# Kernel optimization log

Hardware: AMD Instinct MI355X
Metric: run time of the kernel (lower is better)

Reference implementation:

```python
import jax, jax.numpy as jnp
import numpy as np

N = 20000        # nodes
E = 320000       # edges (avg degree 16)
F_IN = 128       # node_features
F2 = 64          # second_features (per-head out dim, LSTM hidden)
H = 8            # heads
D1 = H * F2      # 512, concat output of GATConv / LSTM input
NEG_SLOPE = 0.2  # GATConv default leaky_relu slope


def _gat_conv(x, src, dst, W, att_src, att_dst, bias):
    """PyG GATConv (concat=True, self-loops added, eval-mode dropout)."""
    n = x.shape[0]
    h = (x @ W).reshape(n, H, -1)                      # [N,H,F]
    a_s = (h * att_src).sum(-1)                        # [N,H]
    a_d = (h * att_dst).sum(-1)                        # [N,H]
    e = jax.nn.leaky_relu(a_s[src] + a_d[dst], NEG_SLOPE)   # [E',H]
    m = jax.ops.segment_max(e, dst, num_segments=n)    # [N,H]
    m = jnp.where(jnp.isfinite(m), m, 0.0)
    ex = jnp.exp(e - m[dst])
    denom = jax.ops.segment_sum(ex, dst, num_segments=n)
    alpha = ex / (denom[dst] + 1e-16)                  # [E',H]
    msg = h[src] * alpha[:, :, None]                   # [E',H,F]
    out = jax.ops.segment_sum(msg, dst, num_segments=n)  # [N,H,F]
    return out.reshape(n, -1) + bias                   # [N,H*F]


def _lstm_step(x, W_ih, W_hh, b_ih, b_hh):
    """Single-timestep PyTorch LSTM with zero initial (h0, c0). x: [N,D1]."""
    h0 = jnp.zeros((x.shape[0], F2), x.dtype)
    gates = x @ W_ih.T + b_ih + h0 @ W_hh.T + b_hh     # [N,4*F2]
    i, f, g, o = jnp.split(gates, 4, axis=-1)
    c = jax.nn.sigmoid(f) * 0.0 + jax.nn.sigmoid(i) * jnp.tanh(g)
    h = jax.nn.sigmoid(o) * jnp.tanh(c)
    return h, (h, c)


def setup_inputs() -> dict:
    key = jax.random.key(0)
    ks = jax.random.split(key, 16)

    def glorot(k, shape, fan_in):
        return jax.random.normal(k, shape, jnp.float32) * (1.0 / np.sqrt(fan_in))

    return {
        "x": jax.random.normal(ks[0], (N, F_IN), jnp.float32),
        "edge_index": jax.random.randint(ks[1], (2, E), 0, N, jnp.int32),
        "edge_weight": jax.random.uniform(ks[2], (E,), jnp.float32),
        # GATConv 1: F_IN -> H*F2
        "W1": glorot(ks[3], (F_IN, H * F2), F_IN),
        "att_src1": glorot(ks[4], (H, F2), F2),
        "att_dst1": glorot(ks[5], (H, F2), F2),
        "bias1": jnp.zeros((H * F2,), jnp.float32),
        # LSTM: input D1 -> hidden F2
        "W_ih": glorot(ks[6], (4 * F2, D1), D1),
        "W_hh": glorot(ks[7], (4 * F2, F2), F2),
        "b_ih": jnp.zeros((4 * F2,), jnp.float32),
        "b_hh": jnp.zeros((4 * F2,), jnp.float32),
        # GATConv 2: F2 -> H*F2
        "W2": glorot(ks[8], (F2, H * F2), F2),
        "att_src2": glorot(ks[9], (H, F2), F2),
        "att_dst2": glorot(ks[10], (H, F2), F2),
        "bias2": jnp.zeros((H * F2,), jnp.float32),
    }


def reference(x, edge_index, edge_weight, W1, att_src1, att_dst1, bias1,
              W_ih, W_hh, b_ih, b_hh, W2, att_src2, att_dst2, bias2):
    # edge_weight is accepted but unused, matching the original forward.
    loops = jnp.arange(N, dtype=edge_index.dtype)
    src = jnp.concatenate([edge_index[0], loops])      # add self-loops (PyG default)
    dst = jnp.concatenate([edge_index[1], loops])

    h = _gat_conv(x, src, dst, W1, att_src1, att_dst1, bias1)   # [N,512]
    h, hidden2 = _lstm_step(h, W_ih, W_hh, b_ih, b_hh)          # [N,64]
    h = jax.nn.relu(h)
    h = _gat_conv(h, src, dst, W2, att_src2, att_dst2, bias2)   # [N,512]
    return jax.nn.softmax(h, axis=1)
```

## Files before the change

kernel.cpp:

```cpp
#include <hip/hip_runtime.h>
#include <math.h>


__global__ void count_kernel(const int* __restrict__ dst, int* __restrict__ deg, int E) {
  int i = blockIdx.x * 256 + threadIdx.x;
  if (i < E) atomicAdd(&deg[dst[i]], 1);
}

__global__ void scan_kernel(const int* __restrict__ deg, int* __restrict__ rowptr, int n) {
  __shared__ int buf[1024];
  __shared__ int carry;
  if (threadIdx.x == 0) carry = 0;
  __syncthreads();
  for (int base = 0; base < n; base += 8192) {
    int v[8];
    int tsum = 0;
    int i0 = base + (int)threadIdx.x * 8;
#pragma unroll
    for (int k = 0; k < 8; ++k) {
      int i = i0 + k;
      v[k] = (i < n) ? (deg[i] + 1) : 0;
      tsum += v[k];
    }
    int incl = tsum;
    buf[threadIdx.x] = incl;
    __syncthreads();
    for (int s = 1; s < 1024; s <<= 1) {
      int t = (threadIdx.x >= (unsigned)s) ? buf[threadIdx.x - s] : 0;
      __syncthreads();
      incl += t;
      buf[threadIdx.x] = incl;
      __syncthreads();
    }
    int excl = carry + incl - tsum;
#pragma unroll
    for (int k = 0; k < 8; ++k) {
      int i = i0 + k;
      if (i < n) rowptr[i] = excl;
      excl += v[k];
    }
    int total = buf[1023];
    __syncthreads();
    if (threadIdx.x == 0) carry += total;
    __syncthreads();
  }
  if (threadIdx.x == 0) rowptr[n] = carry;
}

__global__ void scatter_kernel(const int* __restrict__ src, const int* __restrict__ dst,
                               const int* __restrict__ rowptr, int* __restrict__ wp,
                               int* __restrict__ col, int E, int n) {
  int i = blockIdx.x * 256 + threadIdx.x;
  if (i < E) {
    int d = dst[i];
    int p = rowptr[d] + atomicAdd(&wp[d], 1);
    col[p] = src[i];
  } else if (i < E + n) {
    int d = i - E;
    int p = rowptr[d] + atomicAdd(&wp[d], 1);
    col[p] = d;
  }
}


template <int BMt>
__global__ __launch_bounds__(256) void gemm_kernel(
    const float* __restrict__ A, const float* __restrict__ B,
    float* __restrict__ C, const float* __restrict__ bias,
    int M, int K, int lda, int ldb, int ldc,
    int aZ, int bZ, int cZ, int biasZ) {
  constexpr int BNt = 64, BKt = 16;
  constexpr int TM = BMt / 16;
  constexpr int AST = (BMt * BKt) / (256 * 4);
  __shared__ float As[BKt][BMt + 4];
  __shared__ float Bs[BKt][BNt];
  const int z = blockIdx.z;
  A += (size_t)z * aZ;
  B += (size_t)z * bZ;
  C += (size_t)z * cZ;
  const int tid = threadIdx.x;
  const int bm = blockIdx.y * BMt;
  const int bn = blockIdx.x * BNt;
  const int tm = (tid >> 4) * TM;
  const int tn = (tid & 15) * 4;
  int arow_[AST], akq_[AST];
#pragma unroll
  for (int i = 0; i < AST; ++i) {
    int idx = tid + i * 256;
    arow_[i] = idx >> 2;
    akq_[i] = (idx & 3) * 4;
  }
  const int bk = tid >> 4, bn4 = (tid & 15) * 4;
  float4 pa[AST], pb;
#pragma unroll
  for (int i = 0; i < AST; ++i) {
    pa[i] = make_float4(0.f, 0.f, 0.f, 0.f);
    if (bm + arow_[i] < M)
      pa[i] = *reinterpret_cast<const float4*>(A + (size_t)(bm + arow_[i]) * lda + akq_[i]);
  }
  pb = *reinterpret_cast<const float4*>(B + (size_t)bk * ldb + bn + bn4);
  float acc[TM][4] = {};
  for (int k0 = 0; k0 < K; k0 += BKt) {
#pragma unroll
    for (int i = 0; i < AST; ++i) {
      As[akq_[i] + 0][arow_[i]] = pa[i].x; As[akq_[i] + 1][arow_[i]] = pa[i].y;
      As[akq_[i] + 2][arow_[i]] = pa[i].z; As[akq_[i] + 3][arow_[i]] = pa[i].w;
    }
    *reinterpret_cast<float4*>(&Bs[bk][bn4]) = pb;
    __syncthreads();
    const int kn = k0 + BKt;
    if (kn < K) {
#pragma unroll
      for (int i = 0; i < AST; ++i) {
        float4 t = make_float4(0.f, 0.f, 0.f, 0.f);
        if (bm + arow_[i] < M)
          t = *reinterpret_cast<const float4*>(A + (size_t)(bm + arow_[i]) * lda + kn + akq_[i]);
        pa[i] = t;
      }
      pb = *reinterpret_cast<const float4*>(B + (size_t)(kn + bk) * ldb + bn + bn4);
    }
#pragma unroll
    for (int k = 0; k < BKt; ++k) {
      float a[TM], b[4];
#pragma unroll
      for (int i = 0; i < TM; ++i) a[i] = As[k][tm + i];
#pragma unroll
      for (int j = 0; j < 4; ++j) b[j] = Bs[k][tn + j];
#pragma unroll
      for (int i = 0; i < TM; ++i)
#pragma unroll
        for (int j = 0; j < 4; ++j) acc[i][j] = fmaf(a[i], b[j], acc[i][j]);
    }
    __syncthreads();
  }
  float4 bz = make_float4(0.f, 0.f, 0.f, 0.f);
  if (bias) bz = *reinterpret_cast<const float4*>(bias + (size_t)z * biasZ + bn + tn);
#pragma unroll
  for (int i = 0; i < TM; ++i) {
    int m = bm + tm + i;
    if (m < M) {
      float4 o;
      o.x = acc[i][0] + bz.x; o.y = acc[i][1] + bz.y;
      o.z = acc[i][2] + bz.z; o.w = acc[i][3] + bz.w;
      *reinterpret_cast<float4*>(C + (size_t)m * ldc + bn + tn) = o;
    }
  }
}


__global__ void prep_all_kernel(const float* __restrict__ W_ih, const float* __restrict__ b_ih,
                                const float* __restrict__ b_hh, const float* __restrict__ W1,
                                const float* __restrict__ as1, const float* __restrict__ ad1,
                                const float* __restrict__ W2, const float* __restrict__ as2,
                                const float* __restrict__ ad2, float* __restrict__ Wt,
                                float* __restrict__ bsum, float* __restrict__ watt1,
                                float* __restrict__ watt2) {
  int idx = blockIdx.x * 256 + threadIdx.x;
  if (idx < 98304) {
    int k = idx / 192, jp = idx - k * 192;
    int j = (jp < 64) ? jp : jp + 64;
    Wt[idx] = W_ih[(size_t)j * 512 + k];
  } else if (idx < 98496) {
    int jp = idx - 98304;
    int j = (jp < 64) ? jp : jp + 64;
    bsum[jp] = b_ih[j] + b_hh[j];
  } else if (idx < 100544) {
    int t = idx - 98496;
    int f = t >> 4, c = t & 15;
    int k = c & 7;
    const float* att = ((c < 8) ? as1 : ad1) + k * 64;
    const float* w = W1 + (size_t)f * 512 + k * 64;
    float s = 0.f;
#pragma unroll
    for (int j = 0; j < 64; ++j) s = fmaf(w[j], att[j], s);
    watt1[t] = s;
  } else if (idx < 101568) {
    int t = idx - 100544;
    int f = t >> 4, c = t & 15;
    int k = c & 7;
    const float* att = ((c < 8) ? as2 : ad2) + k * 64;
    const float* w = W2 + (size_t)f * 512 + k * 64;
    float s = 0.f;
#pragma unroll
    for (int j = 0; j < 64; ++j) s = fmaf(w[j], att[j], s);
    watt2[t] = s;
  }
}


template <int F>
__global__ __launch_bounds__(256) void attcoef_kernel(
    const float* __restrict__ feat, const float* __restrict__ watt,
    float* __restrict__ a_s, float* __restrict__ a_d, int n) {
  __shared__ float rows[16 * F];
  __shared__ float wbuf[F * 16];
  const int n0 = blockIdx.x * 16;
  const int tid = threadIdx.x;
  if (n0 + 16 <= n) {
    const float4* g = reinterpret_cast<const float4*>(feat + (size_t)n0 * F);
    float4* l = reinterpret_cast<float4*>(rows);
    for (int i = tid; i < 16 * F / 4; i += 256) l[i] = g[i];
  } else {
    for (int i = tid; i < 16 * F; i += 256) {
      int r = i / F;
      rows[i] = (n0 + r < n) ? feat[(size_t)(n0 + r) * F + (i - r * F)] : 0.f;
    }
  }
  {
    const float4* g = reinterpret_cast<const float4*>(watt);
    float4* l = reinterpret_cast<float4*>(wbuf);
    for (int i = tid; i < F * 16 / 4; i += 256) l[i] = g[i];
  }
  __syncthreads();
  const int local = tid >> 4, c = tid & 15;
  float s = 0.f;
#pragma unroll 8
  for (int f = 0; f < F; ++f) s = fmaf(rows[local * F + f], wbuf[f * 16 + c], s);
  const int node = n0 + local;
  if (node < n) {
    if (c < 8) a_s[(size_t)node * 8 + c] = s;
    else       a_d[(size_t)node * 8 + (c - 8)] = s;
  }
}


template <int F>
__global__ __launch_bounds__(256) void gat_aggregate_wave(
    const float* __restrict__ feat, const float* __restrict__ a_s,
    const float* __restrict__ a_d, const int* __restrict__ rowptr,
    const int* __restrict__ col, float* __restrict__ agg, int n) {
  constexpr int F4 = F / 4;
  constexpr int HPG = (F == 128) ? 4 : 2;
  __shared__ float s_alpha[4][8][8];
  __shared__ int s_cols[4][8];
  const int wid = threadIdx.x >> 6;
  const int lane = threadIdx.x & 63;
  const int node = blockIdx.x * 4 + wid;
  if (node >= n) return;
  const int start = rowptr[node];
  const int deg = rowptr[node + 1] - start;
  const int j = lane >> 3;
  const int h = lane & 7;
  const float adh = a_d[(size_t)node * 8 + h];
  float den = 0.f;
  for (int e = j; e < deg; e += 8) {
    int s = col[start + e];
    float v = a_s[(size_t)s * 8 + h] + adh;
    v = (v > 0.f) ? v : 0.2f * v;
    den += __expf(v);
  }
  den += __shfl_xor(den, 8);
  den += __shfl_xor(den, 16);
  den += __shfl_xor(den, 32);
  const float inv = 1.f / (den + 1e-16f);
  const int f4 = lane & (F4 - 1);
  const int hbase = (lane / F4) * HPG;
  float4 acc0 = make_float4(0.f, 0.f, 0.f, 0.f);
  float4 acc1 = make_float4(0.f, 0.f, 0.f, 0.f);
  float4 acc2 = make_float4(0.f, 0.f, 0.f, 0.f);
  float4 acc3 = make_float4(0.f, 0.f, 0.f, 0.f);
  for (int c0 = 0; c0 < deg; c0 += 8) {
    float aval = 0.f;
    int sj = 0;
    if (c0 + j < deg) {
      sj = col[start + c0 + j];
      float v = a_s[(size_t)sj * 8 + h] + adh;
      v = (v > 0.f) ? v : 0.2f * v;
      aval = __expf(v) * inv;
    }
    s_alpha[wid][j][h] = aval;
    if (h == 0) s_cols[wid][j] = sj;
    __builtin_amdgcn_wave_barrier();
    const int ce = min(8, deg - c0);
    for (int e = 0; e < ce; ++e) {
      int s = s_cols[wid][e];
      float4 fv = *reinterpret_cast<const float4*>(feat + (size_t)s * F + f4 * 4);
      if constexpr (HPG == 4) {
        float4 al = *reinterpret_cast<const float4*>(&s_alpha[wid][e][hbase]);
        acc0.x = fmaf(al.x, fv.x, acc0.x); acc0.y = fmaf(al.x, fv.y, acc0.y);
        acc0.z = fmaf(al.x, fv.z, acc0.z); acc0.w = fmaf(al.x, fv.w, acc0.w);
        acc1.x = fmaf(al.y, fv.x, acc1.x); acc1.y = fmaf(al.y, fv.y, acc1.y);
        acc1.z = fmaf(al.y, fv.z, acc1.z); acc1.w = fmaf(al.y, fv.w, acc1.w);
        acc2.x = fmaf(al.z, fv.x, acc2.x); acc2.y = fmaf(al.z, fv.y, acc2.y);
        acc2.z = fmaf(al.z, fv.z, acc2.z); acc2.w = fmaf(al.z, fv.w, acc2.w);
        acc3.x = fmaf(al.w, fv.x, acc3.x); acc3.y = fmaf(al.w, fv.y, acc3.y);
        acc3.z = fmaf(al.w, fv.z, acc3.z); acc3.w = fmaf(al.w, fv.w, acc3.w);
      } else {
        float2 al = *reinterpret_cast<const float2*>(&s_alpha[wid][e][hbase]);
        acc0.x = fmaf(al.x, fv.x, acc0.x); acc0.y = fmaf(al.x, fv.y, acc0.y);
        acc0.z = fmaf(al.x, fv.z, acc0.z); acc0.w = fmaf(al.x, fv.w, acc0.w);
        acc1.x = fmaf(al.y, fv.x, acc1.x); acc1.y = fmaf(al.y, fv.y, acc1.y);
        acc1.z = fmaf(al.y, fv.z, acc1.z); acc1.w = fmaf(al.y, fv.w, acc1.w);
      }
    }
    __builtin_amdgcn_wave_barrier();
  }
  float* outp = agg + (size_t)node * 8 * F + (size_t)hbase * F + f4 * 4;
  *reinterpret_cast<float4*>(outp) = acc0;
  *reinterpret_cast<float4*>(outp + F) = acc1;
  if constexpr (HPG == 4) {
    *reinterpret_cast<float4*>(outp + 2 * F) = acc2;
    *reinterpret_cast<float4*>(outp + 3 * F) = acc3;
  }
}


__global__ __launch_bounds__(256) void lstm_act_attcoef_kernel(
    const float* __restrict__ gp0, const float* __restrict__ bsum,
    const float* __restrict__ watt2, float* __restrict__ h2,
    float* __restrict__ a_s2, float* __restrict__ a_d2, int n) {
  __shared__ float h2t[4][64];
  __shared__ float wbuf[64 * 16];
  const int tid = threadIdx.x;
  reinterpret_cast<float4*>(wbuf)[tid] = reinterpret_cast<const float4*>(watt2)[tid];
  const int nl = tid >> 6, j = tid & 63;
  const int node = blockIdx.x * 4 + nl;
  const float* gp1 = gp0 + (size_t)n * 192;
  float hv = 0.f;
  if (node < n) {
    const float* g0 = gp0 + (size_t)node * 192;
    const float* g1 = gp1 + (size_t)node * 192;
    float iv = g0[j] + g1[j] + bsum[j];
    float gv = g0[64 + j] + g1[64 + j] + bsum[64 + j];
    float ov = g0[128 + j] + g1[128 + j] + bsum[128 + j];
    float c = (1.f / (1.f + __expf(-iv))) * tanhf(gv);
    hv = fmaxf((1.f / (1.f + __expf(-ov))) * tanhf(c), 0.f);
    h2[(size_t)node * 64 + j] = hv;
  }
  h2t[nl][j] = hv;
  __syncthreads();
  if (j < 16 && node < n) {
    float s = 0.f;
#pragma unroll 16
    for (int f = 0; f < 64; ++f) s = fmaf(h2t[nl][f], wbuf[f * 16 + j], s);
    if (j < 8) a_s2[(size_t)node * 8 + j] = s;
    else       a_d2[(size_t)node * 8 + (j - 8)] = s;
  }
}


__global__ __launch_bounds__(256) void softmax512_wave(const float* __restrict__ in,
                                                       float* __restrict__ out, int n) {
  const int wid = threadIdx.x >> 6, lane = threadIdx.x & 63;
  const int node = blockIdx.x * 4 + wid;
  if (node >= n) return;
  const float4* ip = reinterpret_cast<const float4*>(in + (size_t)node * 512);
  float4 v0 = ip[lane];
  float4 v1 = ip[64 + lane];
  float m = fmaxf(fmaxf(fmaxf(v0.x, v0.y), fmaxf(v0.z, v0.w)),
                  fmaxf(fmaxf(v1.x, v1.y), fmaxf(v1.z, v1.w)));
#pragma unroll
  for (int d = 1; d < 64; d <<= 1) m = fmaxf(m, __shfl_xor(m, d));
  float4 e0, e1;
  e0.x = __expf(v0.x - m); e0.y = __expf(v0.y - m);
  e0.z = __expf(v0.z - m); e0.w = __expf(v0.w - m);
  e1.x = __expf(v1.x - m); e1.y = __expf(v1.y - m);
  e1.z = __expf(v1.z - m); e1.w = __expf(v1.w - m);
  float s = e0.x + e0.y + e0.z + e0.w + e1.x + e1.y + e1.z + e1.w;
#pragma unroll
  for (int d = 1; d < 64; d <<= 1) s += __shfl_xor(s, d);
  float inv = 1.f / s;
  e0.x *= inv; e0.y *= inv; e0.z *= inv; e0.w *= inv;
  e1.x *= inv; e1.y *= inv; e1.z *= inv; e1.w *= inv;
  float4* op = reinterpret_cast<float4*>(out + (size_t)node * 512);
  op[lane] = e0;
  op[64 + lane] = e1;
}


extern "C" void kernel_launch(void* const* d_in, const int* in_sizes, int n_in,
                              void* d_out, int out_size, void* d_ws, size_t ws_size,
                              hipStream_t stream) {
  const float* x      = (const float*)d_in[0];
  const int*   ei     = (const int*)d_in[1];
  const float* W1     = (const float*)d_in[3];
  const float* att_s1 = (const float*)d_in[4];
  const float* att_d1 = (const float*)d_in[5];
  const float* bias1  = (const float*)d_in[6];
  const float* W_ih   = (const float*)d_in[7];
  const float* b_ih   = (const float*)d_in[9];
  const float* b_hh   = (const float*)d_in[10];
  const float* W2     = (const float*)d_in[11];
  const float* att_s2 = (const float*)d_in[12];
  const float* att_d2 = (const float*)d_in[13];
  const float* bias2  = (const float*)d_in[14];
  float* out = (float*)d_out;

  const int N = in_sizes[0] / 128;
  const int E = in_sizes[1] / 2;
  const int* src = ei;
  const int* dst = ei + E;

  char* p = (char*)d_ws;
  auto alloc = [&](size_t bytes) {
    char* r = p;
    p += (bytes + 255) & ~(size_t)255;
    return r;
  };
  float* slotA = (float*)alloc((size_t)N * 1024 * 4);
  float* slotB = (float*)alloc((size_t)N * 512 * 4);
  float* a_s1 = (float*)alloc((size_t)N * 8 * 4);
  float* a_d1 = (float*)alloc((size_t)N * 8 * 4);
  float* a_s2 = (float*)alloc((size_t)N * 8 * 4);
  float* a_d2 = (float*)alloc((size_t)N * 8 * 4);
  float* watt1 = (float*)alloc(128 * 16 * 4);
  float* watt2 = (float*)alloc(64 * 16 * 4);
  float* Wt   = (float*)alloc((size_t)512 * 192 * 4);
  float* bsum = (float*)alloc(192 * 4);
  int* deg    = (int*)alloc((size_t)2 * N * 4);
  int* wp     = deg + N;
  int* rowptr = (int*)alloc((size_t)(N + 1) * 4);
  int* col    = (int*)alloc((size_t)(E + N) * 4);

  float* agg1   = slotA;
  float* g1     = slotB;
  float* gates2 = slotA;
  float* h2     = slotA + (size_t)N * 384;
  float* agg2   = slotA + (size_t)N * 448;
  float* h3p    = slotB;

  hipMemsetAsync(deg, 0, (size_t)2 * N * 4, stream);
  count_kernel<<<(E + 255) / 256, 256, 0, stream>>>(dst, deg, E);
  scan_kernel<<<1, 1024, 0, stream>>>(deg, rowptr, N);
  scatter_kernel<<<(E + N + 255) / 256, 256, 0, stream>>>(src, dst, rowptr, wp, col, E, N);

  prep_all_kernel<<<(101568 + 255) / 256, 256, 0, stream>>>(
      W_ih, b_ih, b_hh, W1, att_s1, att_d1, W2, att_s2, att_d2,
      Wt, bsum, watt1, watt2);

  attcoef_kernel<128><<<(N + 15) / 16, 256, 0, stream>>>(x, watt1, a_s1, a_d1, N);
  gat_aggregate_wave<128><<<(N + 3) / 4, 256, 0, stream>>>(x, a_s1, a_d1, rowptr, col, agg1, N);
  {
    dim3 g(1, (N + 127) / 128, 8);
    gemm_kernel<128><<<g, 256, 0, stream>>>(agg1, W1, g1, bias1,
                                            N, 128, 1024, 512, 512, 128, 64, 64, 64);
  }

  {
    dim3 g(3, (N + 63) / 64, 2);
    gemm_kernel<64><<<g, 256, 0, stream>>>(g1, Wt, gates2, nullptr,
                                           N, 256, 512, 192, 192,
                                           256, 256 * 192, N * 192, 0);
  }
  lstm_act_attcoef_kernel<<<(N + 3) / 4, 256, 0, stream>>>(gates2, bsum, watt2,
                                                           h2, a_s2, a_d2, N);

  gat_aggregate_wave<64><<<(N + 3) / 4, 256, 0, stream>>>(h2, a_s2, a_d2, rowptr, col, agg2, N);
  {
    dim3 g(1, (N + 127) / 128, 8);
    gemm_kernel<128><<<g, 256, 0, stream>>>(agg2, W2, h3p, bias2,
                                            N, 64, 512, 512, 512, 64, 64, 64, 64);
  }
  softmax512_wave<<<(N + 3) / 4, 256, 0, stream>>>(h3p, out, N);
}
```

Measured before the change: 388.4 us.

## Fold W1 into LSTM input weights and fuse two GEMMs into one

Precomputes a fused weight matrix (per-head W1 slice times W_ih) so the aggregated features go straight to LSTM gates through a single K=1024 GEMM. This removes the intermediate g1 buffer and one GEMM launch, and folds bias1 into the gate bias. The GEMM gets wider N tiles (192 columns), and the K dimension is split into 2 or 4 parts depending on workspace size. It also drops the memset by zeroing degrees in the prep kernel and simplifies the scan to a single pass. In exchange the K split adds partial-sum traffic and the FLOP count rises from K=128+512 to K=1024 per node.

```diff
diff --git a/kernel.cpp b/kernel.cpp
--- a/kernel.cpp
+++ b/kernel.cpp
@@ -9,42 +9,34 @@
 
 __global__ void scan_kernel(const int* __restrict__ deg, int* __restrict__ rowptr, int n) {
   __shared__ int buf[1024];
-  __shared__ int carry;
-  if (threadIdx.x == 0) carry = 0;
+  const int tid = threadIdx.x;
+  const int i0 = tid * 20;
+  int v[20];
+  int tsum = 0;
+#pragma unroll
+  for (int k = 0; k < 20; ++k) {
+    int i = i0 + k;
+    v[k] = (i < n) ? (deg[i] + 1) : 0;
+    tsum += v[k];
+  }
+  int incl = tsum;
+  buf[tid] = incl;
   __syncthreads();
-  for (int base = 0; base < n; base += 8192) {
-    int v[8];
-    int tsum = 0;
-    int i0 = base + (int)threadIdx.x * 8;
-#pragma unroll
-    for (int k = 0; k < 8; ++k) {
-      int i = i0 + k;
-      v[k] = (i < n) ? (deg[i] + 1) : 0;
-      tsum += v[k];
-    }
-    int incl = tsum;
-    buf[threadIdx.x] = incl;
+  for (int s = 1; s < 1024; s <<= 1) {
+    int t = (tid >= (unsigned)s) ? buf[tid - s] : 0;
     __syncthreads();
-    for (int s = 1; s < 1024; s <<= 1) {
-      int t = (threadIdx.x >= (unsigned)s) ? buf[threadIdx.x - s] : 0;
-      __syncthreads();
-      incl += t;
-      buf[threadIdx.x] = incl;
-      __syncthreads();
-    }
-    int excl = carry + incl - tsum;
-#pragma unroll
-    for (int k = 0; k < 8; ++k) {
-      int i = i0 + k;
-      if (i < n) rowptr[i] = excl;
-      excl += v[k];
-    }
-    int total = buf[1023];
+    incl += t;
+    buf[tid] = incl;
     __syncthreads();
-    if (threadIdx.x == 0) carry += total;
-    __syncthreads();
-  }
-  if (threadIdx.x == 0) rowptr[n] = carry;
+  }
+  int excl = incl - tsum;
+#pragma unroll
+  for (int k = 0; k < 20; ++k) {
+    int i = i0 + k;
+    if (i < n) rowptr[i] = excl;
+    excl += v[k];
+  }
+  if (tid == 1023) rowptr[n] = incl;
 }
 
 __global__ void scatter_kernel(const int* __restrict__ src, const int* __restrict__ dst,
@@ -63,15 +55,17 @@
 }
 
 
-template <int BMt>
+template <int BMt, int BNt, int TNt>
 __global__ __launch_bounds__(256) void gemm_kernel(
     const float* __restrict__ A, const float* __restrict__ B,
     float* __restrict__ C, const float* __restrict__ bias,
     int M, int K, int lda, int ldb, int ldc,
     int aZ, int bZ, int cZ, int biasZ) {
-  constexpr int BNt = 64, BKt = 16;
+  constexpr int BKt = 16;
   constexpr int TM = BMt / 16;
-  constexpr int AST = (BMt * BKt) / (256 * 4);
+  constexpr int AST = (BMt * BKt) / 1024;
+  constexpr int BST = (BKt * BNt) / 1024;
+  static_assert(BNt == 16 * TNt, "layout");
   __shared__ float As[BKt][BMt + 4];
   __shared__ float Bs[BKt][BNt];
   const int z = blockIdx.z;
@@ -82,7 +76,7 @@
   const int bm = blockIdx.y * BMt;
   const int bn = blockIdx.x * BNt;
   const int tm = (tid >> 4) * TM;
-  const int tn = (tid & 15) * 4;
+  const int tn = (tid & 15) * TNt;
   int arow_[AST], akq_[AST];
 #pragma unroll
   for (int i = 0; i < AST; ++i) {
@@ -90,23 +84,33 @@
     arow_[i] = idx >> 2;
     akq_[i] = (idx & 3) * 4;
   }
-  const int bk = tid >> 4, bn4 = (tid & 15) * 4;
-  float4 pa[AST], pb;
+  int bkr_[BST], bc4_[BST];
+#pragma unroll
+  for (int i = 0; i < BST; ++i) {
+    int idx = tid + i * 256;
+    bkr_[i] = idx / (BNt / 4);
+    bc4_[i] = (idx % (BNt / 4)) * 4;
+  }
+  float4 pa[AST], pb[BST];
 #pragma unroll
   for (int i = 0; i < AST; ++i) {
     pa[i] = make_float4(0.f, 0.f, 0.f, 0.f);
     if (bm + arow_[i] < M)
       pa[i] = *reinterpret_cast<const float4*>(A + (size_t)(bm + arow_[i]) * lda + akq_[i]);
   }
-  pb = *reinterpret_cast<const float4*>(B + (size_t)bk * ldb + bn + bn4);
-  float acc[TM][4] = {};
+#pragma unroll
+  for (int i = 0; i < BST; ++i)
+    pb[i] = *reinterpret_cast<const float4*>(B + (size_t)bkr_[i] * ldb + bn + bc4_[i]);
+  float acc[TM][TNt] = {};
   for (int k0 = 0; k0 < K; k0 += BKt) {
 #pragma unroll
     for (int i = 0; i < AST; ++i) {
       As[akq_[i] + 0][arow_[i]] = pa[i].x; As[akq_[i] + 1][arow_[i]] = pa[i].y;
       As[akq_[i] + 2][arow_[i]] = pa[i].z; As[akq_[i] + 3][arow_[i]] = pa[i].w;
     }
-    *reinterpret_cast<float4*>(&Bs[bk][bn4]) = pb;
+#pragma unroll
+    for (int i = 0; i < BST; ++i)
+      *reinterpret_cast<float4*>(&Bs[bkr_[i]][bc4_[i]]) = pb[i];
     __syncthreads();
     const int kn = k0 + BKt;
     if (kn < K) {
@@ -117,55 +121,82 @@
           t = *reinterpret_cast<const float4*>(A + (size_t)(bm + arow_[i]) * lda + kn + akq_[i]);
         pa[i] = t;
       }
-      pb = *reinterpret_cast<const float4*>(B + (size_t)(kn + bk) * ldb + bn + bn4);
+#pragma unroll
+      for (int i = 0; i < BST; ++i)
+        pb[i] = *reinterpret_cast<const float4*>(B + (size_t)(kn + bkr_[i]) * ldb + bn + bc4_[i]);
     }
 #pragma unroll
     for (int k = 0; k < BKt; ++k) {
-      float a[TM], b[4];
+      float a[TM], b[TNt];
 #pragma unroll
       for (int i = 0; i < TM; ++i) a[i] = As[k][tm + i];
 #pragma unroll
-      for (int j = 0; j < 4; ++j) b[j] = Bs[k][tn + j];
+      for (int q = 0; q < TNt / 4; ++q) {
+        float4 bv = *reinterpret_cast<const float4*>(&Bs[k][tn + q * 4]);
+        b[q * 4 + 0] = bv.x; b[q * 4 + 1] = bv.y;
+        b[q * 4 + 2] = bv.z; b[q * 4 + 3] = bv.w;
+      }
 #pragma unroll
       for (int i = 0; i < TM; ++i)
 #pragma unroll
-        for (int j = 0; j < 4; ++j) acc[i][j] = fmaf(a[i], b[j], acc[i][j]);
+        for (int j = 0; j < TNt; ++j) acc[i][j] = fmaf(a[i], b[j], acc[i][j]);
     }
     __syncthreads();
   }
-  float4 bz = make_float4(0.f, 0.f, 0.f, 0.f);
-  if (bias) bz = *reinterpret_cast<const float4*>(bias + (size_t)z * biasZ + bn + tn);
+  float bz[TNt];
+#pragma unroll
+  for (int j = 0; j < TNt; ++j) bz[j] = 0.f;
+  if (bias) {
+#pragma unroll
+    for (int q = 0; q < TNt / 4; ++q) {
+      float4 bv = *reinterpret_cast<const float4*>(bias + (size_t)z * biasZ + bn + tn + q * 4);
+      bz[q * 4 + 0] = bv.x; bz[q * 4 + 1] = bv.y;
+      bz[q * 4 + 2] = bv.z; bz[q * 4 + 3] = bv.w;
+    }
+  }
 #pragma unroll
   for (int i = 0; i < TM; ++i) {
     int m = bm + tm + i;
     if (m < M) {
-      float4 o;
-      o.x = acc[i][0] + bz.x; o.y = acc[i][1] + bz.y;
-      o.z = acc[i][2] + bz.z; o.w = acc[i][3] + bz.w;
-      *reinterpret_cast<float4*>(C + (size_t)m * ldc + bn + tn) = o;
+#pragma unroll
+      for (int q = 0; q < TNt / 4; ++q) {
+        float4 o;
+        o.x = acc[i][q * 4 + 0] + bz[q * 4 + 0];
+        o.y = acc[i][q * 4 + 1] + bz[q * 4 + 1];
+        o.z = acc[i][q * 4 + 2] + bz[q * 4 + 2];
+        o.w = acc[i][q * 4 + 3] + bz[q * 4 + 3];
+        *reinterpret_cast<float4*>(C + (size_t)m * ldc + bn + tn + q * 4) = o;
+      }
     }
   }
 }
 
 
 __global__ void prep_all_kernel(const float* __restrict__ W_ih, const float* __restrict__ b_ih,
-                                const float* __restrict__ b_hh, const float* __restrict__ W1,
+                                const float* __restrict__ b_hh, const float* __restrict__ bias1,
+                                const float* __restrict__ W1,
                                 const float* __restrict__ as1, const float* __restrict__ ad1,
                                 const float* __restrict__ W2, const float* __restrict__ as2,
-                                const float* __restrict__ ad2, float* __restrict__ Wt,
-                                float* __restrict__ bsum, float* __restrict__ watt1,
-                                float* __restrict__ watt2) {
+                                const float* __restrict__ ad2,
+                                int* __restrict__ degwp, float* __restrict__ bsum,
+                                float* __restrict__ watt1, float* __restrict__ watt2,
+                                float* __restrict__ Wfused, int n2) {
   int idx = blockIdx.x * 256 + threadIdx.x;
-  if (idx < 98304) {
-    int k = idx / 192, jp = idx - k * 192;
-    int j = (jp < 64) ? jp : jp + 64;
-    Wt[idx] = W_ih[(size_t)j * 512 + k];
-  } else if (idx < 98496) {
-    int jp = idx - 98304;
-    int j = (jp < 64) ? jp : jp + 64;
-    bsum[jp] = b_ih[j] + b_hh[j];
-  } else if (idx < 100544) {
-    int t = idx - 98496;
+  if (idx < n2) {
+    degwp[idx] = 0;
+    return;
+  }
+  int t = idx - n2;
+  if (t < 192) {
+    int j = (t < 64) ? t : t + 64;
+    float s = b_ih[j] + b_hh[j];
+    const float* w = W_ih + (size_t)j * 512;
+    for (int k = 0; k < 512; ++k) s = fmaf(bias1[k], w[k], s);
+    bsum[t] = s;
+    return;
+  }
+  t -= 192;
+  if (t < 2048) {
     int f = t >> 4, c = t & 15;
     int k = c & 7;
     const float* att = ((c < 8) ? as1 : ad1) + k * 64;
@@ -174,8 +205,10 @@
 #pragma unroll
     for (int j = 0; j < 64; ++j) s = fmaf(w[j], att[j], s);
     watt1[t] = s;
-  } else if (idx < 101568) {
-    int t = idx - 100544;
+    return;
+  }
+  t -= 2048;
+  if (t < 1024) {
     int f = t >> 4, c = t & 15;
     int k = c & 7;
     const float* att = ((c < 8) ? as2 : ad2) + k * 64;
@@ -184,6 +217,19 @@
 #pragma unroll
     for (int j = 0; j < 64; ++j) s = fmaf(w[j], att[j], s);
     watt2[t] = s;
+    return;
+  }
+  t -= 1024;
+  if (t < 196608) {
+    int hr = t / 192, jp = t - hr * 192;
+    int h = hr >> 7, r = hr & 127;
+    int j = (jp < 64) ? jp : jp + 64;
+    const float* w1 = W1 + (size_t)r * 512 + h * 64;
+    const float* wi = W_ih + (size_t)j * 512 + h * 64;
+    float s = 0.f;
+#pragma unroll
+    for (int c = 0; c < 64; ++c) s = fmaf(w1[c], wi[c], s);
+    Wfused[(size_t)hr * 192 + jp] = s;
   }
 }
 
@@ -308,21 +354,28 @@
 __global__ __launch_bounds__(256) void lstm_act_attcoef_kernel(
     const float* __restrict__ gp0, const float* __restrict__ bsum,
     const float* __restrict__ watt2, float* __restrict__ h2,
-    float* __restrict__ a_s2, float* __restrict__ a_d2, int n) {
+    float* __restrict__ a_s2, float* __restrict__ a_d2, int n, int nsplit) {
   __shared__ float h2t[4][64];
   __shared__ float wbuf[64 * 16];
   const int tid = threadIdx.x;
   reinterpret_cast<float4*>(wbuf)[tid] = reinterpret_cast<const float4*>(watt2)[tid];
   const int nl = tid >> 6, j = tid & 63;
   const int node = blockIdx.x * 4 + nl;
-  const float* gp1 = gp0 + (size_t)n * 192;
   float hv = 0.f;
   if (node < n) {
     const float* g0 = gp0 + (size_t)node * 192;
-    const float* g1 = gp1 + (size_t)node * 192;
-    float iv = g0[j] + g1[j] + bsum[j];
-    float gv = g0[64 + j] + g1[64 + j] + bsum[64 + j];
-    float ov = g0[128 + j] + g1[128 + j] + bsum[128 + j];
+    const float* g1 = g0 + (size_t)n * 192;
+    float iv = g0[j] + g1[j];
+    float gv = g0[64 + j] + g1[64 + j];
+    float ov = g0[128 + j] + g1[128 + j];
+    if (nsplit == 4) {
+      const float* g2 = g1 + (size_t)n * 192;
+      const float* g3 = g2 + (size_t)n * 192;
+      iv += g2[j] + g3[j];
+      gv += g2[64 + j] + g3[64 + j];
+      ov += g2[128 + j] + g3[128 + j];
+    }
+    iv += bsum[j]; gv += bsum[64 + j]; ov += bsum[128 + j];
     float c = (1.f / (1.f + __expf(-iv))) * tanhf(gv);
     hv = fmaxf((1.f / (1.f + __expf(-ov))) * tanhf(c), 0.f);
     h2[(size_t)node * 64 + j] = hv;
@@ -391,6 +444,22 @@
   const int* src = ei;
   const int* dst = ei + E;
 
+  auto total_ws = [&](int slotBfloats) {
+    size_t s = 0;
+    auto add = [&](size_t b) { s += (b + 255) & ~(size_t)255; };
+    add((size_t)N * 1024 * 4);
+    add((size_t)slotBfloats * 4);
+    add((size_t)N * 8 * 4); add((size_t)N * 8 * 4);
+    add((size_t)N * 8 * 4); add((size_t)N * 8 * 4);
+    add(128 * 16 * 4); add(64 * 16 * 4);
+    add((size_t)1024 * 192 * 4); add(192 * 4);
+    add((size_t)2 * N * 4); add((size_t)(N + 1) * 4); add((size_t)(E + N) * 4);
+    return s;
+  };
+  const int slotB4 = (int)((size_t)N * 768 > (size_t)N * 512 ? (size_t)N * 768 : (size_t)N * 512);
+  const int nsplit = (total_ws(slotB4) <= ws_size) ? 4 : 2;
+  const int slotBfloats = (nsplit == 4) ? slotB4 : (int)((size_t)N * 512);
+
   char* p = (char*)d_ws;
   auto alloc = [&](size_t bytes) {
     char* r = p;
@@ -398,14 +467,14 @@
     return r;
   };
   float* slotA = (float*)alloc((size_t)N * 1024 * 4);
-  float* slotB = (float*)alloc((size_t)N * 512 * 4);
+  float* slotB = (float*)alloc((size_t)slotBfloats * 4);
   float* a_s1 = (float*)alloc((size_t)N * 8 * 4);
   float* a_d1 = (float*)alloc((size_t)N * 8 * 4);
   float* a_s2 = (float*)alloc((size_t)N * 8 * 4);
   float* a_d2 = (float*)alloc((size_t)N * 8 * 4);
   float* watt1 = (float*)alloc(128 * 16 * 4);
   float* watt2 = (float*)alloc(64 * 16 * 4);
-  float* Wt   = (float*)alloc((size_t)512 * 192 * 4);
+  float* Wfused = (float*)alloc((size_t)1024 * 192 * 4);
   float* bsum = (float*)alloc(192 * 4);
   int* deg    = (int*)alloc((size_t)2 * N * 4);
   int* wp     = deg + N;
@@ -413,43 +482,40 @@
   int* col    = (int*)alloc((size_t)(E + N) * 4);
 
   float* agg1   = slotA;
-  float* g1     = slotB;
-  float* gates2 = slotA;
-  float* h2     = slotA + (size_t)N * 384;
-  float* agg2   = slotA + (size_t)N * 448;
+  float* gatesP = slotB;
+  float* h2     = slotA;
+  float* agg2   = slotA + (size_t)N * 64;
   float* h3p    = slotB;
 
-  hipMemsetAsync(deg, 0, (size_t)2 * N * 4, stream);
+  {
+    int total = 2 * N + 192 + 2048 + 1024 + 196608;
+    prep_all_kernel<<<(total + 255) / 256, 256, 0, stream>>>(
+        W_ih, b_ih, b_hh, bias1, W1, att_s1, att_d1, W2, att_s2, att_d2,
+        deg, bsum, watt1, watt2, Wfused, 2 * N);
+  }
+
   count_kernel<<<(E + 255) / 256, 256, 0, stream>>>(dst, deg, E);
   scan_kernel<<<1, 1024, 0, stream>>>(deg, rowptr, N);
   scatter_kernel<<<(E + N + 255) / 256, 256, 0, stream>>>(src, dst, rowptr, wp, col, E, N);
 
-  prep_all_kernel<<<(101568 + 255) / 256, 256, 0, stream>>>(
-      W_ih, b_ih, b_hh, W1, att_s1, att_d1, W2, att_s2, att_d2,
-      Wt, bsum, watt1, watt2);
-
   attcoef_kernel<128><<<(N + 15) / 16, 256, 0, stream>>>(x, watt1, a_s1, a_d1, N);
   gat_aggregate_wave<128><<<(N + 3) / 4, 256, 0, stream>>>(x, a_s1, a_d1, rowptr, col, agg1, N);
+
   {
-    dim3 g(1, (N + 127) / 128, 8);
-    gemm_kernel<128><<<g, 256, 0, stream>>>(agg1, W1, g1, bias1,
-                                            N, 128, 1024, 512, 512, 128, 64, 64, 64);
-  }
-
-  {
-    dim3 g(3, (N + 63) / 64, 2);
-    gemm_kernel<64><<<g, 256, 0, stream>>>(g1, Wt, gates2, nullptr,
-                                           N, 256, 512, 192, 192,
-                                           256, 256 * 192, N * 192, 0);
-  }
-  lstm_act_attcoef_kernel<<<(N + 3) / 4, 256, 0, stream>>>(gates2, bsum, watt2,
-                                                           h2, a_s2, a_d2, N);
+    int Kz = 1024 / nsplit;
+    dim3 g(1, (N + 63) / 64, nsplit);
+    gemm_kernel<64, 192, 12><<<g, 256, 0, stream>>>(agg1, Wfused, gatesP, nullptr,
+                                                    N, Kz, 1024, 192, 192,
+                                                    Kz, Kz * 192, N * 192, 0);
+  }
+  lstm_act_attcoef_kernel<<<(N + 3) / 4, 256, 0, stream>>>(gatesP, bsum, watt2,
+                                                           h2, a_s2, a_d2, N, nsplit);
 
   gat_aggregate_wave<64><<<(N + 3) / 4, 256, 0, stream>>>(h2, a_s2, a_d2, rowptr, col, agg2, N);
   {
     dim3 g(1, (N + 127) / 128, 8);
-    gemm_kernel<128><<<g, 256, 0, stream>>>(agg2, W2, h3p, bias2,
-                                            N, 64, 512, 512, 512, 64, 64, 64, 64);
+    gemm_kernel<128, 64, 4><<<g, 256, 0, stream>>>(agg2, W2, h3p, bias2,
+                                                   N, 64, 512, 512, 512, 64, 64, 64, 64);
   }
   softmax512_wave<<<(N + 3) / 4, 256, 0, stream>>>(h3p, out, N);
 }
```

After: 415.2 us. 6.9% more time.
